# Optimization experiments

Hardware: AMD Instinct MI355X
Metric: run time of the kernel (lower is better)

## Reference

```python
import jax, jax.numpy as jnp
import numpy as np

B, CIN, COUT, H, W = 8, 64, 64, 256, 256
M1, M2, NPROD = 16, 16, 4
COUT_LIN = COUT - NPROD  # 60
SCALE = 1.0 / (CIN * COUT)


def setup_inputs() -> dict:
    key = jax.random.key(0)
    ks = jax.random.split(key, 5)
    wshape = (CIN, COUT_LIN, M1, M2)
    return {
        "x": jax.random.normal(ks[0], (B, CIN, H, W), dtype=jnp.float32),
        "w1r": SCALE * jax.random.uniform(ks[1], wshape, dtype=jnp.float32),
        "w1i": SCALE * jax.random.uniform(ks[2], wshape, dtype=jnp.float32),
        "w2r": SCALE * jax.random.uniform(ks[3], wshape, dtype=jnp.float32),
        "w2i": SCALE * jax.random.uniform(ks[4], wshape, dtype=jnp.float32),
    }


def reference(x, w1r, w1i, w2r, w2i):
    b, c, h, w = x.shape
    wf = w // 2 + 1  # rfft width
    w1 = w1r + 1j * w1i
    w2 = w2r + 1j * w2i

    x_ft = jnp.fft.rfft2(x)  # [b, c, h, wf] complex64

    # mode-truncated channel mixing on low / high frequency blocks
    low = jnp.einsum("bixy,ioxy->boxy", x_ft[:, :, :M1, :M2], w1)
    high = jnp.einsum("bixy,ioxy->boxy", x_ft[:, :, h - M1:, :M2], w2)

    out_ft = jnp.zeros((b, COUT_LIN, h, wf), dtype=x_ft.dtype)
    out_ft = out_ft.at[:, :, :M1, :M2].set(low)
    out_ft = out_ft.at[:, :, h - M1:, :M2].set(high)

    # product path: complex pairwise products of adjacent channels
    prod = out_ft[:, 0:2 * NPROD:2] * out_ft[:, 1:2 * NPROD:2]  # [b, NPROD, h, wf]
    out_ft_full = jnp.concatenate([out_ft, prod], axis=1)  # [b, COUT, h, wf]

    return jnp.fft.irfft2(out_ft_full, s=(h, w))  # [b, COUT, h, w] real
```

## Files before the change

kernel.cpp:

```cpp
#include <hip/hip_runtime.h>

#define TWOPI_256 0.024543692606170259f

typedef __attribute__((ext_vector_type(8))) short bf16x8;
typedef __attribute__((ext_vector_type(4))) float f32x4;

__device__ __forceinline__ unsigned int bfp(float a) {
  return (__float_as_uint(a) + 0x8000u) >> 16;
}
__device__ __forceinline__ float bf2f(unsigned int h) {
  return __uint_as_float(h << 16);
}

__global__ __launch_bounds__(256) void k1_fwd(const float* __restrict__ x,
                                              float2* __restrict__ Xm) {
  const int blk = blockIdx.x;
  const int tid = threadIdx.x;
  const int lane = tid & 63;
  const int wv = tid >> 6;
  const int llo = lane & 15;
  const int lhi = lane >> 4;

  __shared__ float tabc[256];
  __shared__ float tabs[256];
  __shared__ short EbRH[16][264];
  __shared__ short EbRL[16][264];
  __shared__ short EbIH[16][264];
  __shared__ short EbIL[16][264];
  __shared__ short XbH[32][264];
  __shared__ short XbL[32][264];
  __shared__ float Pbf[8704];

  const float4* xb4 = (const float4*)(x + ((size_t)blk << 16));
  float4 vld[8];
#pragma unroll
  for (int q = 0; q < 8; ++q) vld[q] = xb4[q * 256 + tid];

  {
    float s, c;
    sincosf((float)tid * TWOPI_256, &s, &c);
    tabc[tid] = c;
    tabs[tid] = s;
  }
  __syncthreads();

  {
    const int w = tid;
#pragma unroll
    for (int kk = 0; kk < 16; ++kk) {
      const int idx = (kk * w) & 255;
      const float cv = tabc[idx];
      const float sv = -tabs[idx];
      const unsigned hc = bfp(cv);
      const unsigned hs = bfp(sv);
      const unsigned lc = bfp(cv - bf2f(hc));
      const unsigned ls = bfp(sv - bf2f(hs));
      EbRH[kk][w] = (short)hc;
      EbRL[kk][w] = (short)lc;
      EbIH[kk][w] = (short)hs;
      EbIL[kk][w] = (short)ls;
    }
  }

  for (int c = 0; c < 8; ++c) {
#pragma unroll
    for (int q = 0; q < 8; ++q) {
      const int row = q * 4 + wv;
      const float4 v = vld[q];
      const unsigned h0 = bfp(v.x), h1 = bfp(v.y), h2 = bfp(v.z), h3 = bfp(v.w);
      const unsigned l0 = bfp(v.x - bf2f(h0)), l1 = bfp(v.y - bf2f(h1));
      const unsigned l2 = bfp(v.z - bf2f(h2)), l3 = bfp(v.w - bf2f(h3));
      const int sb = (tid & 63) * 4;
      *(uint2*)&XbH[row][sb] = make_uint2(h0 | (h1 << 16), h2 | (h3 << 16));
      *(uint2*)&XbL[row][sb] = make_uint2(l0 | (l1 << 16), l2 | (l3 << 16));
    }
    __syncthreads();
    if (c < 7) {
#pragma unroll
      for (int q = 0; q < 8; ++q) vld[q] = xb4[(c + 1) * 2048 + q * 256 + tid];
    }
    if (wv < 2) {
      f32x4 cre = {0.f, 0.f, 0.f, 0.f};
      f32x4 cim = {0.f, 0.f, 0.f, 0.f};
#pragma unroll
      for (int ks = 0; ks < 8; ++ks) {
        const int wb = ks * 32 + lhi * 8;
        const bf16x8 aH = *(const bf16x8*)&XbH[wv * 16 + llo][wb];
        const bf16x8 aL = *(const bf16x8*)&XbL[wv * 16 + llo][wb];
        const bf16x8 bRH = *(const bf16x8*)&EbRH[llo][wb];
        const bf16x8 bRL = *(const bf16x8*)&EbRL[llo][wb];
        const bf16x8 bIH = *(const bf16x8*)&EbIH[llo][wb];
        const bf16x8 bIL = *(const bf16x8*)&EbIL[llo][wb];
        cre = __builtin_amdgcn_mfma_f32_16x16x32_bf16(aH, bRH, cre, 0, 0, 0);
        cre = __builtin_amdgcn_mfma_f32_16x16x32_bf16(aL, bRH, cre, 0, 0, 0);
        cre = __builtin_amdgcn_mfma_f32_16x16x32_bf16(aH, bRL, cre, 0, 0, 0);
        cim = __builtin_amdgcn_mfma_f32_16x16x32_bf16(aH, bIH, cim, 0, 0, 0);
        cim = __builtin_amdgcn_mfma_f32_16x16x32_bf16(aL, bIH, cim, 0, 0, 0);
        cim = __builtin_amdgcn_mfma_f32_16x16x32_bf16(aH, bIL, cim, 0, 0, 0);
      }
#pragma unroll
      for (int r = 0; r < 4; ++r) {
        const int h = c * 32 + wv * 16 + lhi * 4 + r;
        *(float2*)&Pbf[llo * 544 + 4 * (llo & 7) + 2 * h] =
            make_float2(cre[r], cim[r]);
      }
    }
    __syncthreads();
  }

  const int k = tid & 15;
  const int tt = tid >> 4;
  const int pbase = k * 544 + 4 * (k & 7);
  float c0 = 1.f, s0 = 0.f, c1 = 1.f, s1 = 0.f;
  const float cr0 = tabc[tt], sr0 = tabs[tt];
  const float cr1 = tabc[240 + tt], sr1 = tabs[240 + tt];
  float X0r = 0.f, X0i = 0.f, X1r = 0.f, X1i = 0.f;
  for (int h = 0; h < 256; h += 2) {
    const float4 pv = *(const float4*)&Pbf[pbase + 2 * h];
    X0r += pv.x * c0 + pv.y * s0; X0i += pv.y * c0 - pv.x * s0;
    X1r += pv.x * c1 + pv.y * s1; X1i += pv.y * c1 - pv.x * s1;
    float cn = c0 * cr0 - s0 * sr0, sn = s0 * cr0 + c0 * sr0; c0 = cn; s0 = sn;
    cn = c1 * cr1 - s1 * sr1; sn = s1 * cr1 + c1 * sr1; c1 = cn; s1 = sn;
    X0r += pv.z * c0 + pv.w * s0; X0i += pv.w * c0 - pv.z * s0;
    X1r += pv.z * c1 + pv.w * s1; X1i += pv.w * c1 - pv.z * s1;
    cn = c0 * cr0 - s0 * sr0; sn = s0 * cr0 + c0 * sr0; c0 = cn; s0 = sn;
    cn = c1 * cr1 - s1 * sr1; sn = s1 * cr1 + c1 * sr1; c1 = cn; s1 = sn;
  }
  const int ci = blk & 63, b = blk >> 6;
  Xm[((tt * 16 + k) * 64 + ci) * 8 + b]        = make_float2(X0r, X0i);
  Xm[(((tt + 16) * 16 + k) * 64 + ci) * 8 + b] = make_float2(X1r, X1i);
}

__global__ __launch_bounds__(256) void k2_mix(const float2* __restrict__ Xm,
                                              const float* __restrict__ w1r,
                                              const float* __restrict__ w1i,
                                              const float* __restrict__ w2r,
                                              const float* __restrict__ w2i,
                                              float2* __restrict__ Am) {
  const int blk = blockIdx.x;
  const int t = blk >> 4, k = blk & 15;
  const int tp = t & 15;
  const float* __restrict__ wr = (t < 16) ? w1r : w2r;
  const float* __restrict__ wi = (t < 16) ? w1i : w2i;
  const int tid = threadIdx.x;

  __shared__ float2 Xs[64][8];
  __shared__ float2 Cb[64][8];

  {
    const float2* src = Xm + ((size_t)blk << 9);
    float2* dst = &Xs[0][0];
    dst[tid] = src[tid];
    dst[tid + 256] = src[tid + 256];
  }
  __syncthreads();

  for (int n = tid; n < 480; n += 256) {
    const int o = n >> 3, bb = n & 7;
    const int wofs = o * 256 + tp * 16 + k;
    float ar = 0.f, ai = 0.f;
#pragma unroll 4
    for (int i = 0; i < 64; ++i) {
      const float wrv = wr[i * 15360 + wofs];
      const float wiv = wi[i * 15360 + wofs];
      const float2 xv = Xs[i][bb];
      ar += xv.x * wrv - xv.y * wiv;
      ai += xv.x * wiv + xv.y * wrv;
    }
    Cb[o][bb] = make_float2(ar, ai);
  }
  __syncthreads();
  if (tid < 32) {
    const int p = tid >> 3, bb = tid & 7;
    const float2 u = Cb[2 * p][bb], v = Cb[2 * p + 1][bb];
    Cb[60 + p][bb] = make_float2(u.x * v.x - u.y * v.y, u.x * v.y + u.y * v.x);
  }
  __syncthreads();
  const float alpha = (k == 0 ? 1.f : 2.f) * (1.f / 65536.f);
#pragma unroll
  for (int n = tid; n < 512; n += 256) {
    const int o = n >> 3, bb = n & 7;
    const float2 v = Cb[o][bb];
    Am[(((size_t)(bb * 64 + o)) * 32 + t) * 16 + k] = make_float2(v.x * alpha, v.y * alpha);
  }
}

__global__ __launch_bounds__(256) void k3_inv(const float2* __restrict__ Am,
                                              float* __restrict__ out) {
  const int blk = blockIdx.x;
  const int tid = threadIdx.x;
  const int lane = tid & 63, wv = tid >> 6;
  const int llo = lane & 15, lhi = lane >> 4;

  __shared__ float tabc[256];
  __shared__ float tabs[256];
  __shared__ float2 Ams[32][16];
  __shared__ short Zh[256][40];
  __shared__ short TbH[256][40];
  __shared__ short TbL[256][40];

  {
    float s, c;
    sincosf((float)tid * TWOPI_256, &s, &c);
    tabc[tid] = c;
    tabs[tid] = s;
  }
  {
    const float2* src = Am + ((size_t)blk << 9);
    float2* dst = &Ams[0][0];
    dst[tid] = src[tid];
    dst[tid + 256] = src[tid + 256];
  }
  __syncthreads();

  {
    const int w = tid;
#pragma unroll
    for (int t = 0; t < 16; ++t) {
      const int idx = (t * w) & 255;
      const float cv = tabc[idx], sv = -tabs[idx];
      const unsigned hc = bfp(cv), hs = bfp(sv);
      const unsigned lc = bfp(cv - bf2f(hc)), ls = bfp(sv - bf2f(hs));
      *(unsigned*)&TbH[w][2 * t] = hc | (hs << 16);
      *(unsigned*)&TbL[w][2 * t] = lc | (ls << 16);
    }
  }

  const int hg = tid >> 2, kg = tid & 3;
  float Zr[4][4], Zi[4][4];
#pragma unroll
  for (int i = 0; i < 4; ++i)
#pragma unroll
    for (int j = 0; j < 4; ++j) { Zr[i][j] = 0.f; Zi[i][j] = 0.f; }
  float ch[4], sh[4], crh[4], srh[4];
#pragma unroll
  for (int i = 0; i < 4; ++i) {
    const int h = hg * 4 + i;
    crh[i] = tabc[h];
    srh[i] = tabs[h];
    ch[i] = 1.f;
    sh[i] = 0.f;
  }
  for (int t = 0; t < 32; ++t) {
    if (t == 16) {
#pragma unroll
      for (int i = 0; i < 4; ++i) {
        const int idx = (240 * (hg * 4 + i)) & 255;
        ch[i] = tabc[idx];
        sh[i] = tabs[idx];
      }
    }
    const float4 a01 = *(const float4*)&Ams[t][kg * 4];
    const float4 a23 = *(const float4*)&Ams[t][kg * 4 + 2];
    const float Ar[4] = {a01.x, a01.z, a23.x, a23.z};
    const float Ai[4] = {a01.y, a01.w, a23.y, a23.w};
#pragma unroll
    for (int i = 0; i < 4; ++i) {
#pragma unroll
      for (int j = 0; j < 4; ++j) {
        Zr[i][j] += Ar[j] * ch[i] - Ai[j] * sh[i];
        Zi[i][j] += Ar[j] * sh[i] + Ai[j] * ch[i];
      }
      const float cn = ch[i] * crh[i] - sh[i] * srh[i];
      const float sn = sh[i] * crh[i] + ch[i] * srh[i];
      ch[i] = cn;
      sh[i] = sn;
    }
  }
#pragma unroll
  for (int j = 0; j < 4; ++j) {
#pragma unroll
    for (int i = 0; i < 4; ++i) {
      const int kk = kg * 4 + j, h = hg * 4 + i;
      *(unsigned*)&Zh[h][2 * kk] = bfp(Zr[i][j]) | (bfp(Zi[i][j]) << 16);
    }
  }
  __syncthreads();

  float* op = out + ((size_t)blk << 16);
#pragma unroll
  for (int hti = 0; hti < 4; ++hti) {
    const int h0 = (wv * 4 + hti) * 16;
    const bf16x8 za = *(const bf16x8*)&Zh[h0 + llo][lhi * 8];
    const int rbase = (h0 + lhi * 4) * 256 + llo;
#pragma unroll 4
    for (int wt = 0; wt < 16; ++wt) {
      const bf16x8 th = *(const bf16x8*)&TbH[wt * 16 + llo][lhi * 8];
      const bf16x8 tl = *(const bf16x8*)&TbL[wt * 16 + llo][lhi * 8];
      f32x4 acc = {0.f, 0.f, 0.f, 0.f};
      acc = __builtin_amdgcn_mfma_f32_16x16x32_bf16(za, th, acc, 0, 0, 0);
      acc = __builtin_amdgcn_mfma_f32_16x16x32_bf16(za, tl, acc, 0, 0, 0);
#pragma unroll
      for (int r = 0; r < 4; ++r) op[rbase + r * 256 + wt * 16] = acc[r];
    }
  }
}

extern "C" void kernel_launch(void* const* d_in, const int* in_sizes, int n_in,
                              void* d_out, int out_size, void* d_ws, size_t ws_size,
                              hipStream_t stream) {
  const float* x   = (const float*)d_in[0];
  const float* w1r = (const float*)d_in[1];
  const float* w1i = (const float*)d_in[2];
  const float* w2r = (const float*)d_in[3];
  const float* w2i = (const float*)d_in[4];
  float* out = (float*)d_out;

  float2* Xm = (float2*)d_ws;
  float2* Am = Xm + 262144;

  k1_fwd<<<dim3(512), dim3(256), 0, stream>>>(x, Xm);
  k2_mix<<<dim3(512), dim3(256), 0, stream>>>(Xm, w1r, w1i, w2r, w2i, Am);
  k3_inv<<<dim3(512), dim3(256), 0, stream>>>(Am, out);
}
```

Before: 319.6 us.

## Split forward kernel, stage mix weights in LDS, vectorize inverse output stores

The forward kernel is split in two. The first does the MFMA width-DFT and writes partial results to a workspace. The second reloads them and does the height-DFT, so each kernel needs less LDS and can keep more blocks resident. The mixing kernel now loads its per-mode weight slice into shared memory once instead of reading strided global memory in the inner loop. The inverse kernel swaps the MFMA operand order so each lane writes contiguous float4 rows instead of scalar strided stores. In exchange it adds an extra kernel launch and a workspace round trip of about 16 MB.

```diff
diff --git a/kernel.cpp b/kernel.cpp
--- a/kernel.cpp
+++ b/kernel.cpp
@@ -12,8 +12,8 @@
   return __uint_as_float(h << 16);
 }
 
-__global__ __launch_bounds__(256) void k1_fwd(const float* __restrict__ x,
-                                              float2* __restrict__ Xm) {
+__global__ __launch_bounds__(256) void k1a_fwd(const float* __restrict__ x,
+                                               float2* __restrict__ Pws) {
   const int blk = blockIdx.x;
   const int tid = threadIdx.x;
   const int lane = tid & 63;
@@ -29,7 +29,6 @@
   __shared__ short EbIL[16][264];
   __shared__ short XbH[32][264];
   __shared__ short XbL[32][264];
-  __shared__ float Pbf[8704];
 
   const float4* xb4 = (const float4*)(x + ((size_t)blk << 16));
   float4 vld[8];
@@ -98,15 +97,41 @@
         cim = __builtin_amdgcn_mfma_f32_16x16x32_bf16(aL, bIH, cim, 0, 0, 0);
         cim = __builtin_amdgcn_mfma_f32_16x16x32_bf16(aH, bIL, cim, 0, 0, 0);
       }
-#pragma unroll
-      for (int r = 0; r < 4; ++r) {
-        const int h = c * 32 + wv * 16 + lhi * 4 + r;
-        *(float2*)&Pbf[llo * 544 + 4 * (llo & 7) + 2 * h] =
-            make_float2(cre[r], cim[r]);
-      }
+      const int h0 = c * 32 + wv * 16 + lhi * 4;
+      float4* p = (float4*)(Pws + ((size_t)blk * 4096 + llo * 256 + h0));
+      p[0] = make_float4(cre[0], cim[0], cre[1], cim[1]);
+      p[1] = make_float4(cre[2], cim[2], cre[3], cim[3]);
     }
     __syncthreads();
   }
+}
+
+__global__ __launch_bounds__(256) void k1b_fwd(const float2* __restrict__ Pws,
+                                               float2* __restrict__ Xm) {
+  const int blk = blockIdx.x;
+  const int tid = threadIdx.x;
+
+  __shared__ float tabc[256];
+  __shared__ float tabs[256];
+  __shared__ float Pbf[8704];
+
+  {
+    float s, c;
+    sincosf((float)tid * TWOPI_256, &s, &c);
+    tabc[tid] = c;
+    tabs[tid] = s;
+  }
+  {
+    const float4* src = (const float4*)(Pws + (size_t)blk * 4096);
+#pragma unroll
+    for (int q = 0; q < 8; ++q) {
+      const int vIdx = q * 256 + tid;
+      const float4 v = src[vIdx];
+      const int k = vIdx >> 7, h2 = vIdx & 127;
+      *(float4*)&Pbf[k * 544 + 4 * (k & 7) + 4 * h2] = v;
+    }
+  }
+  __syncthreads();
 
   const int k = tid & 15;
   const int tt = tid >> 4;
@@ -144,6 +169,8 @@
   const float* __restrict__ wi = (t < 16) ? w1i : w2i;
   const int tid = threadIdx.x;
 
+  __shared__ float Wr[3840];
+  __shared__ float Wi[3840];
   __shared__ float2 Xs[64][8];
   __shared__ float2 Cb[64][8];
 
@@ -153,16 +180,24 @@
     dst[tid] = src[tid];
     dst[tid + 256] = src[tid + 256];
   }
+  {
+    const int base = tp * 16 + k;
+    for (int n = tid; n < 3840; n += 256) {
+      const int i = n / 60, o = n - i * 60;
+      const int a = i * 15360 + o * 256 + base;
+      Wr[n] = wr[a];
+      Wi[n] = wi[a];
+    }
+  }
   __syncthreads();
 
   for (int n = tid; n < 480; n += 256) {
     const int o = n >> 3, bb = n & 7;
-    const int wofs = o * 256 + tp * 16 + k;
     float ar = 0.f, ai = 0.f;
-#pragma unroll 4
+#pragma unroll 8
     for (int i = 0; i < 64; ++i) {
-      const float wrv = wr[i * 15360 + wofs];
-      const float wiv = wi[i * 15360 + wofs];
+      const float wrv = Wr[i * 60 + o];
+      const float wiv = Wi[i * 60 + o];
       const float2 xv = Xs[i][bb];
       ar += xv.x * wrv - xv.y * wiv;
       ai += xv.x * wiv + xv.y * wrv;
@@ -281,17 +316,16 @@
 #pragma unroll
   for (int hti = 0; hti < 4; ++hti) {
     const int h0 = (wv * 4 + hti) * 16;
-    const bf16x8 za = *(const bf16x8*)&Zh[h0 + llo][lhi * 8];
-    const int rbase = (h0 + lhi * 4) * 256 + llo;
+    const bf16x8 zb = *(const bf16x8*)&Zh[h0 + llo][lhi * 8];
+    float* rowp = op + (size_t)(h0 + llo) * 256 + lhi * 4;
 #pragma unroll 4
     for (int wt = 0; wt < 16; ++wt) {
       const bf16x8 th = *(const bf16x8*)&TbH[wt * 16 + llo][lhi * 8];
       const bf16x8 tl = *(const bf16x8*)&TbL[wt * 16 + llo][lhi * 8];
       f32x4 acc = {0.f, 0.f, 0.f, 0.f};
-      acc = __builtin_amdgcn_mfma_f32_16x16x32_bf16(za, th, acc, 0, 0, 0);
-      acc = __builtin_amdgcn_mfma_f32_16x16x32_bf16(za, tl, acc, 0, 0, 0);
-#pragma unroll
-      for (int r = 0; r < 4; ++r) op[rbase + r * 256 + wt * 16] = acc[r];
+      acc = __builtin_amdgcn_mfma_f32_16x16x32_bf16(th, zb, acc, 0, 0, 0);
+      acc = __builtin_amdgcn_mfma_f32_16x16x32_bf16(tl, zb, acc, 0, 0, 0);
+      *(float4*)&rowp[wt * 16] = make_float4(acc[0], acc[1], acc[2], acc[3]);
     }
   }
 }
@@ -306,10 +340,12 @@
   const float* w2i = (const float*)d_in[4];
   float* out = (float*)d_out;
 
-  float2* Xm = (float2*)d_ws;
-  float2* Am = Xm + 262144;
-
-  k1_fwd<<<dim3(512), dim3(256), 0, stream>>>(x, Xm);
+  float2* Xm  = (float2*)d_ws;
+  float2* Am  = Xm + 262144;
+  float2* Pws = Am + 262144;
+
+  k1a_fwd<<<dim3(512), dim3(256), 0, stream>>>(x, Pws);
+  k1b_fwd<<<dim3(512), dim3(256), 0, stream>>>(Pws, Xm);
   k2_mix<<<dim3(512), dim3(256), 0, stream>>>(Xm, w1r, w1i, w2r, w2i, Am);
   k3_inv<<<dim3(512), dim3(256), 0, stream>>>(Am, out);
 }
```

Result: slower. 326.6 us (+2.2%).
